# Performance work log

Hardware: AMD Instinct MI355X
Metric: run time of the kernel (lower is better)

Reference implementation:

```python
import jax, jax.numpy as jnp
import numpy as np

N, I, H = 32, 64, 128
B, T = 16, 256


def setup_inputs() -> dict:
    key = jax.random.key(0)
    k1, k2, k3, k4, k5 = jax.random.split(key, 5)
    stdv = 1.0 / np.sqrt(H)
    x = jax.random.normal(k1, (B, T, N * I), dtype=jnp.float32)
    h0 = jnp.zeros((1, B, N * H), dtype=jnp.float32)
    c0 = jnp.zeros((1, B, N * H), dtype=jnp.float32)
    # Block-diagonal weights stored as batched per-block matrices.
    # weight_ih block i is [4H, I], weight_hh block i is [4H, H].
    weight_ih = jax.random.uniform(k2, (N, 4 * H, I), jnp.float32, -stdv, stdv)
    weight_hh = jax.random.uniform(k3, (N, 4 * H, H), jnp.float32, -stdv, stdv)
    bias_ih = jax.random.uniform(k4, (N, 4 * H), jnp.float32, -stdv, stdv)
    bias_hh = jax.random.uniform(k5, (N, 4 * H), jnp.float32, -stdv, stdv)
    return {"x": x, "h0": h0, "c0": c0, "weight_ih": weight_ih,
            "weight_hh": weight_hh, "bias_ih": bias_ih, "bias_hh": bias_hh}


def _wide_lstm(x, h0, c0, weight_ih, weight_hh, bias_ih, bias_hh):
    b, t, _ = x.shape
    xb = x.reshape(b, t, N, I)
    # Precompute input-to-gate projections for all timesteps: [B,T,N,4H]
    gates_x = jnp.einsum('btni,ngi->btng', xb, weight_ih) + bias_ih
    h_t = h0[0].reshape(b, N, H)
    c_t = c0[0].reshape(b, N, H)

    def step(carry, gx_t):
        h, c = carry
        gates_h = jnp.einsum('bnh,ngh->bng', h, weight_hh) + bias_hh
        gates = gx_t + gates_h  # [B,N,4H]
        i_g = jax.nn.sigmoid(gates[..., 0 * H:1 * H])
        f_g = jax.nn.sigmoid(gates[..., 1 * H:2 * H])
        g_g = jnp.tanh(gates[..., 2 * H:3 * H])
        o_g = jax.nn.sigmoid(gates[..., 3 * H:4 * H])
        c_new = f_g * c + i_g * g_g
        h_new = o_g * jnp.tanh(c_new)
        return (h_new, c_new), h_new

    (h_n, c_n), outs = jax.lax.scan(step, (h_t, c_t),
                                    jnp.swapaxes(gates_x, 0, 1))  # scan over T
    output = jnp.swapaxes(outs, 0, 1).reshape(b, t, N * H)
    return output, h_n.reshape(1, b, N * H), c_n.reshape(1, b, N * H)


def reference(x, h0, c0, weight_ih, weight_hh, bias_ih, bias_hh):
    return _wide_lstm(x, h0, c0, weight_ih, weight_hh, bias_ih, bias_hh)
```

## Files before the change

### kernel.cpp

```cpp
#include <hip/hip_runtime.h>
#include <hip/hip_bf16.h>
#include <cstdint>
#include <cstddef>


#define TSTEPS 256

typedef float  f32x4  __attribute__((ext_vector_type(4)));
typedef float  f32x2  __attribute__((ext_vector_type(2)));
typedef __bf16 bf16x8 __attribute__((ext_vector_type(8)));
typedef short  s16x8  __attribute__((ext_vector_type(8)));

union Frag { s16x8 s; bf16x8 b; };

#define KSIG -1.4426950408889634f
#define KTAN  2.8853900817779268f

__device__ __forceinline__ short f2bf(float f) {
  uint32_t u = __builtin_bit_cast(uint32_t, f);
  u += 0x7fffu + ((u >> 16) & 1u);
  return (short)(u >> 16);
}

__device__ __forceinline__ void sync_lds() {
  asm volatile("s_waitcnt lgkmcnt(0)" ::: "memory");
  __builtin_amdgcn_s_barrier();
  asm volatile("" ::: "memory");
}

__device__ __forceinline__ float sig2(float z) {
  return __builtin_amdgcn_rcpf(1.f + __builtin_amdgcn_exp2f(z));
}

__device__ __forceinline__ f32x4 mf(const Frag a, const Frag bb, f32x4 c) {
  return __builtin_amdgcn_mfma_f32_16x16x32_bf16(a.b, bb.b, c, 0, 0, 0);
}

__device__ __forceinline__ float sel4(const f32x4 a, bool m1, bool m2) {
  const float u01 = m1 ? a[1] : a[0];
  const float u23 = m1 ? a[3] : a[2];
  return m2 ? u23 : u01;
}

__global__ __launch_bounds__(1024, 4) void wide_lstm(
    const float* __restrict__ x,   const float* __restrict__ h0,
    const float* __restrict__ c0,  const float* __restrict__ wih,
    const float* __restrict__ whh, const float* __restrict__ bih,
    const float* __restrict__ bhh, float* __restrict__ out)
{
  const int n    = blockIdx.x & 31;
  const int bg   = blockIdx.x >> 5;
  const int tid  = threadIdx.x;
  const int wv   = tid >> 6;
  const int w    = wv & 7;
  const bool isw = (wv < 8);
  const int lane = tid & 63;
  const int col  = lane & 15;
  const int quad = lane >> 4;
  const int b4   = col & 3;
  const int e2   = col >> 2;
  const int hloc = 4 * quad + e2;
  const int hgl  = 16 * w + hloc;
  const int b    = 4 * bg + b4;

  __shared__ alignas(16) short hbuf[2][4 * 144];
  __shared__ alignas(16) short xbuf[2][4 * 96];
  __shared__ alignas(16) float pbuf[8][64][4];

  Frag wfr[3][4];
#pragma unroll
  for (int j = 0; j < 4; ++j) {
    const int g = 128 * j + 16 * w + col;
#pragma unroll
    for (int sl = 0; sl < 3; ++sl) {
      const int s = isw ? sl : sl + 3;
      const int k0 = 32 * s + quad * 8;
      const float* p = (s < 2) ? (wih + (size_t)(n * 512 + g) * 64  + k0)
                               : (whh + (size_t)(n * 512 + g) * 128 + (k0 - 64));
      const f32x4 lo = *(const f32x4*)p;
      const f32x4 hi = *(const f32x4*)(p + 4);
      Frag f;
      f.s[0]=f2bf(lo[0]); f.s[1]=f2bf(lo[1]); f.s[2]=f2bf(lo[2]); f.s[3]=f2bf(lo[3]);
      f.s[4]=f2bf(hi[0]); f.s[5]=f2bf(hi[1]); f.s[6]=f2bf(hi[2]); f.s[7]=f2bf(hi[3]);
      wfr[sl][j] = f;
    }
  }

  const int hoff  = b4 * 144 + quad * 8;
  const int hwoff = b4 * 144 + hgl;
  const int xoff  = b4 * 96  + quad * 8;
  const bool m1 = (e2 & 1), m2 = (e2 & 2);
  const f32x4 kzero = (f32x4){0.f, 0.f, 0.f, 0.f};

  f32x4 cb[4], acpre[4];
  float cg = 0.f, ho = 0.f;
  float* outp = nullptr;
  float xr = 0.f;
  const float* xnext = nullptr;

  if (isw) {
#pragma unroll
    for (int j = 0; j < 4; ++j) {
      const int base = n * 512 + 128 * j + 16 * w + quad * 4;
      const f32x4 b1 = *(const f32x4*)(bih + base);
      const f32x4 b2 = *(const f32x4*)(bhh + base);
#pragma unroll
      for (int r = 0; r < 4; ++r) cb[j][r] = b1[r] + b2[r];
    }
    if (tid < 256) {
      const int bi = tid >> 6, j2 = (tid & 63) * 2;
      const f32x2 hv = *(const f32x2*)(h0 + (size_t)(4 * bg + bi) * 4096 + n * 128 + j2);
      *(uint32_t*)&hbuf[0][bi * 144 + j2] =
          (uint32_t)(uint16_t)f2bf(hv[0]) | ((uint32_t)(uint16_t)f2bf(hv[1]) << 16);
    }
    cg = c0[(size_t)b * 4096 + n * 128 + hgl];
    {
      const float* q = x + (size_t)b * (TSTEPS * 2048) + n * 64 + 8 * quad;
      const f32x4 a0 = *(const f32x4*)q;
      const f32x4 a1 = *(const f32x4*)(q + 4);
      const f32x4 a2 = *(const f32x4*)(q + 32);
      const f32x4 a3 = *(const f32x4*)(q + 36);
      Frag xf0, xf1;
#pragma unroll
      for (int r = 0; r < 4; ++r) {
        xf0.s[r]     = f2bf(a0[r]);
        xf0.s[4 + r] = f2bf(a1[r]);
        xf1.s[r]     = f2bf(a2[r]);
        xf1.s[4 + r] = f2bf(a3[r]);
      }
#pragma unroll
      for (int j = 0; j < 4; ++j)
        acpre[j] = mf(wfr[1][j], xf1, mf(wfr[0][j], xf0, cb[j]));
    }
    outp = out + (size_t)b * (TSTEPS * 4096) + n * 128 + hgl;
  } else if (tid < 768) {
    const int bq = (tid >> 6) & 3;
    const int kq = tid & 63;
    const float* xp = x + (size_t)(4 * bg + bq) * (TSTEPS * 2048) + n * 64 + kq;
    xbuf[1][bq * 96 + kq] = f2bf(xp[2048]);
    xr = xp[2 * 2048];
    xnext = xp + 3 * 2048;
  }
  __syncthreads();

  if (isw) {
#define WSTEP(CUR, NXT, S)                                                   \
  {                                                                          \
    Frag hf0;                                                                \
    hf0.s = *(const s16x8*)&hbuf[CUR][hoff];                                 \
    f32x4 ac1[4];                                                            \
    _Pragma("unroll") for (int j = 0; j < 4; ++j)                            \
      ac1[j] = mf(wfr[2][j], hf0, acpre[j]);                                 \
    float pre[4];                                                            \
    _Pragma("unroll") for (int j = 0; j < 4; ++j)                            \
      pre[j] = sel4(ac1[j], m1, m2);                                         \
    sync_lds();                               \
    const f32x4 vv = *(const f32x4*)&pbuf[w][lane][0];                       \
    pre[0] += vv[0]; pre[1] += vv[1]; pre[2] += vv[2]; pre[3] += vv[3];      \
    const float si = sig2(KSIG * pre[0]);                                    \
    const float sf = sig2(KSIG * pre[1]);                                    \
    const float sg = sig2(KTAN * pre[2]);                                    \
    const float so = sig2(KSIG * pre[3]);                                    \
    float cn = __builtin_fmaf(sf, cg, si);                                   \
    cn = __builtin_fmaf(-2.f, si * sg, cn);                                  \
    cg = cn;                                                                 \
    ho = so * __builtin_fmaf(-2.f, sig2(KTAN * cn), 1.f);                    \
    hbuf[NXT][hwoff] = f2bf(ho);                                             \
    *outp = ho;                                                              \
    outp += 4096;                                                            \
    Frag xg0, xg1;                                                           \
    xg0.s = *(const s16x8*)&xbuf[NXT][xoff];                                 \
    xg1.s = *(const s16x8*)&xbuf[NXT][xoff + 32];                            \
    _Pragma("unroll") for (int j = 0; j < 4; ++j)                            \
      acpre[j] = mf(wfr[0][j], xg0, cb[j]);                                  \
    _Pragma("unroll") for (int j = 0; j < 4; ++j)                            \
      acpre[j] = mf(wfr[1][j], xg1, acpre[j]);                               \
    sync_lds();                                                      \
  }
    for (int t = 0; t < TSTEPS; t += 2) {
      WSTEP(0, 1, t);
      WSTEP(1, 0, t + 1);
    }
#undef WSTEP
    out[16777216 +         (size_t)b * 4096 + n * 128 + hgl] = ho;
    out[16777216 + 65536 + (size_t)b * 4096 + n * 128 + hgl] = cg;
  } else {
    const int sxoff = ((tid >> 6) & 3) * 96 + (tid & 63);
    const bool stg = (tid < 768);
#define VSTEP(CUR, NXT, S)                                                   \
  {                                                                          \
    Frag hf1, hf2, hf3;                                                      \
    hf1.s = *(const s16x8*)&hbuf[CUR][hoff + 32];                            \
    hf2.s = *(const s16x8*)&hbuf[CUR][hoff + 64];                            \
    hf3.s = *(const s16x8*)&hbuf[CUR][hoff + 96];                            \
    if (stg) {                                                               \
      xbuf[CUR][sxoff] = f2bf(xr);                                           \
      if ((S) + 3 < TSTEPS) { xr = *xnext; xnext += 2048; }                  \
    }                                                                        \
    f32x4 ac[4];                                                             \
    _Pragma("unroll") for (int j = 0; j < 4; ++j)                            \
      ac[j] = mf(wfr[0][j], hf1, kzero);                                     \
    _Pragma("unroll") for (int j = 0; j < 4; ++j)                            \
      ac[j] = mf(wfr[1][j], hf2, ac[j]);                                     \
    _Pragma("unroll") for (int j = 0; j < 4; ++j)                            \
      ac[j] = mf(wfr[2][j], hf3, ac[j]);                                     \
    f32x4 vv;                                                                \
    vv[0] = sel4(ac[0], m1, m2);                                             \
    vv[1] = sel4(ac[1], m1, m2);                                             \
    vv[2] = sel4(ac[2], m1, m2);                                             \
    vv[3] = sel4(ac[3], m1, m2);                                             \
    *(f32x4*)&pbuf[w][lane][0] = vv;                                         \
    sync_lds();                                                       \
    sync_lds();                                                      \
  }
    for (int t = 0; t < TSTEPS; t += 2) {
      VSTEP(0, 1, t);
      VSTEP(1, 0, t + 1);
    }
#undef VSTEP
  }
}

extern "C" void kernel_launch(void* const* d_in, const int* in_sizes, int n_in,
                              void* d_out, int out_size, void* d_ws, size_t ws_size,
                              hipStream_t stream) {
  const float* x   = (const float*)d_in[0];
  const float* h0  = (const float*)d_in[1];
  const float* c0  = (const float*)d_in[2];
  const float* wih = (const float*)d_in[3];
  const float* whh = (const float*)d_in[4];
  const float* bih = (const float*)d_in[5];
  const float* bhh = (const float*)d_in[6];
  float* out = (float*)d_out;
  wide_lstm<<<128, 1024, 0, stream>>>(x, h0, c0, wih, whh, bih, bhh, out);
}
```

Before: 267.9 us.

## Precompute input gate projections in a separate GEMM kernel before recurrence

Adds a gx_gemm kernel that computes x·W_ih plus both biases for all timesteps into a workspace buffer. The recurrent kernel then only runs the h·W_hh MFMAs, split evenly between two wave groups, and the helper waves prefetch precomputed gate values four steps ahead. The goal is to take the input projection and x staging off the serial per-step critical path. The cost is an extra kernel launch and a 256 MB fp32 workspace written and read back. The old fused kernel is kept as a fallback when the workspace is too small.

```diff
diff --git a/kernel.cpp b/kernel.cpp
--- a/kernel.cpp
+++ b/kernel.cpp
@@ -42,7 +42,199 @@
   return m2 ? u23 : u01;
 }
 
-__global__ __launch_bounds__(1024, 4) void wide_lstm(
+__global__ __launch_bounds__(512, 2) void gx_gemm(
+    const float* __restrict__ x,   const float* __restrict__ wih,
+    const float* __restrict__ bih, const float* __restrict__ bhh,
+    float* __restrict__ gx)
+{
+  const int n    = blockIdx.x >> 4;
+  const int b    = blockIdx.x & 15;
+  const int tid  = threadIdx.x;
+  const int v    = tid >> 6;
+  const int lane = tid & 63;
+  const int col  = lane & 15;
+  const int quad = lane >> 4;
+
+  Frag wA[4][2];
+#pragma unroll
+  for (int tt = 0; tt < 4; ++tt) {
+    const int g = 128 * (col & 3) + 16 * v + 4 * tt + (col >> 2);
+#pragma unroll
+    for (int s = 0; s < 2; ++s) {
+      const float* p = wih + (size_t)(n * 512 + g) * 64 + 32 * s + quad * 8;
+      const f32x4 lo = *(const f32x4*)p;
+      const f32x4 hi = *(const f32x4*)(p + 4);
+      Frag f;
+      f.s[0]=f2bf(lo[0]); f.s[1]=f2bf(lo[1]); f.s[2]=f2bf(lo[2]); f.s[3]=f2bf(lo[3]);
+      f.s[4]=f2bf(hi[0]); f.s[5]=f2bf(hi[1]); f.s[6]=f2bf(hi[2]); f.s[7]=f2bf(hi[3]);
+      wA[tt][s] = f;
+    }
+  }
+  f32x4 cb[4];
+#pragma unroll
+  for (int tt = 0; tt < 4; ++tt)
+#pragma unroll
+    for (int r = 0; r < 4; ++r) {
+      const int g2 = n * 512 + 128 * r + 16 * v + 4 * tt + quad;
+      cb[tt][r] = bih[g2] + bhh[g2];
+    }
+
+  float* gout = gx + (size_t)(n * 16 + b) * 256 * 512;
+#pragma unroll 2
+  for (int it = 0; it < 16; ++it) {
+    const int t = 16 * it + col;
+    const float* xp = x + ((size_t)b * 256 + t) * 2048 + n * 64;
+    const f32x4 a0 = *(const f32x4*)(xp + 8 * quad);
+    const f32x4 a1 = *(const f32x4*)(xp + 8 * quad + 4);
+    const f32x4 a2 = *(const f32x4*)(xp + 32 + 8 * quad);
+    const f32x4 a3 = *(const f32x4*)(xp + 36 + 8 * quad);
+    Frag xf0, xf1;
+#pragma unroll
+    for (int r = 0; r < 4; ++r) {
+      xf0.s[r]     = f2bf(a0[r]);
+      xf0.s[4 + r] = f2bf(a1[r]);
+      xf1.s[r]     = f2bf(a2[r]);
+      xf1.s[4 + r] = f2bf(a3[r]);
+    }
+#pragma unroll
+    for (int tt = 0; tt < 4; ++tt) {
+      const f32x4 ac = mf(wA[tt][1], xf1, mf(wA[tt][0], xf0, cb[tt]));
+      *(f32x4*)(gout + (size_t)t * 512 + (16 * v + 4 * tt + quad) * 4) = ac;
+    }
+  }
+}
+
+__global__ __launch_bounds__(1024, 2) void wide_lstm_pc(
+    const float* __restrict__ h0,  const float* __restrict__ c0,
+    const float* __restrict__ whh, const float* __restrict__ gx,
+    float* __restrict__ out)
+{
+  const int n    = blockIdx.x & 31;
+  const int bg   = blockIdx.x >> 5;
+  const int tid  = threadIdx.x;
+  const int wv   = tid >> 6;
+  const int w    = wv & 7;
+  const bool isw = (wv < 8);
+  const int lane = tid & 63;
+  const int col  = lane & 15;
+  const int quad = lane >> 4;
+  const int b4   = col & 3;
+  const int e2   = col >> 2;
+  const int hloc = 4 * quad + e2;
+  const int hgl  = 16 * w + hloc;
+  const int b    = 4 * bg + b4;
+
+  __shared__ alignas(16) short hbuf[2][4 * 144];
+  __shared__ alignas(16) float pbuf[8][64][4];
+
+  Frag wfr[2][4];
+#pragma unroll
+  for (int j = 0; j < 4; ++j) {
+    const int g = 128 * j + 16 * w + col;
+#pragma unroll
+    for (int sl = 0; sl < 2; ++sl) {
+      const int k0 = (isw ? 32 * sl : 64 + 32 * sl) + quad * 8;
+      const float* p = whh + (size_t)(n * 512 + g) * 128 + k0;
+      const f32x4 lo = *(const f32x4*)p;
+      const f32x4 hi = *(const f32x4*)(p + 4);
+      Frag f;
+      f.s[0]=f2bf(lo[0]); f.s[1]=f2bf(lo[1]); f.s[2]=f2bf(lo[2]); f.s[3]=f2bf(lo[3]);
+      f.s[4]=f2bf(hi[0]); f.s[5]=f2bf(hi[1]); f.s[6]=f2bf(hi[2]); f.s[7]=f2bf(hi[3]);
+      wfr[sl][j] = f;
+    }
+  }
+
+  const int hoff  = b4 * 144 + quad * 8;
+  const int hwoff = b4 * 144 + hgl;
+  const bool m1 = (e2 & 1), m2 = (e2 & 2);
+  const f32x4 kzero = (f32x4){0.f, 0.f, 0.f, 0.f};
+
+  if (isw) {
+    if (tid < 256) {
+      const int bi = tid >> 6, j2 = (tid & 63) * 2;
+      const f32x2 hv = *(const f32x2*)(h0 + (size_t)(4 * bg + bi) * 4096 + n * 128 + j2);
+      *(uint32_t*)&hbuf[0][bi * 144 + j2] =
+          (uint32_t)(uint16_t)f2bf(hv[0]) | ((uint32_t)(uint16_t)f2bf(hv[1]) << 16);
+    }
+    float cg = c0[(size_t)b * 4096 + n * 128 + hgl];
+    float* outp = out + (size_t)b * (TSTEPS * 4096) + n * 128 + hgl;
+    float ho = 0.f;
+    __syncthreads();
+
+#define WSTEP(CUR, NXT)                                                      \
+  {                                                                          \
+    Frag hf0, hf1;                                                           \
+    hf0.s = *(const s16x8*)&hbuf[CUR][hoff];                                 \
+    hf1.s = *(const s16x8*)&hbuf[CUR][hoff + 32];                            \
+    f32x4 ac1[4];                                                            \
+    _Pragma("unroll") for (int j = 0; j < 4; ++j)                            \
+      ac1[j] = mf(wfr[1][j], hf1, mf(wfr[0][j], hf0, kzero));                \
+    float pre[4];                                                            \
+    _Pragma("unroll") for (int j = 0; j < 4; ++j)                            \
+      pre[j] = sel4(ac1[j], m1, m2);                                         \
+    sync_lds();                      \
+    const f32x4 vv = *(const f32x4*)&pbuf[w][lane][0];                       \
+    pre[0] += vv[0]; pre[1] += vv[1]; pre[2] += vv[2]; pre[3] += vv[3];      \
+    const float si = sig2(KSIG * pre[0]);                                    \
+    const float sf = sig2(KSIG * pre[1]);                                    \
+    const float sg = sig2(KTAN * pre[2]);                                    \
+    const float so = sig2(KSIG * pre[3]);                                    \
+    float cn = __builtin_fmaf(sf, cg, si);                                   \
+    cn = __builtin_fmaf(-2.f, si * sg, cn);                                  \
+    cg = cn;                                                                 \
+    ho = so * __builtin_fmaf(-2.f, sig2(KTAN * cn), 1.f);                    \
+    hbuf[NXT][hwoff] = f2bf(ho);                                             \
+    *outp = ho;                                                              \
+    outp += 4096;                                                            \
+    sync_lds();                                                      \
+  }
+    for (int t = 0; t < TSTEPS; t += 4) {
+      WSTEP(0, 1); WSTEP(1, 0); WSTEP(0, 1); WSTEP(1, 0);
+    }
+#undef WSTEP
+    out[16777216 +         (size_t)b * 4096 + n * 128 + hgl] = ho;
+    out[16777216 + 65536 + (size_t)b * 4096 + n * 128 + hgl] = cg;
+
+  } else {
+    const float* gp = gx + (size_t)(n * 16 + b) * 256 * 512 + hgl * 4;
+    f32x4 g0 = *(const f32x4*)(gp);
+    f32x4 g1 = *(const f32x4*)(gp + 512);
+    f32x4 g2 = *(const f32x4*)(gp + 1024);
+    f32x4 g3 = *(const f32x4*)(gp + 1536);
+    __syncthreads();
+
+#define PSTEP(CUR, NXT, S, GX)                                               \
+  {                                                                          \
+    Frag hf2, hf3;                                                           \
+    hf2.s = *(const s16x8*)&hbuf[CUR][hoff + 64];                            \
+    hf3.s = *(const s16x8*)&hbuf[CUR][hoff + 96];                            \
+    f32x4 ac[4];                                                             \
+    _Pragma("unroll") for (int j = 0; j < 4; ++j)                            \
+      ac[j] = mf(wfr[1][j], hf3, mf(wfr[0][j], hf2, kzero));                 \
+    f32x4 vv;                                                                \
+    vv[0] = sel4(ac[0], m1, m2) + GX[0];                                     \
+    vv[1] = sel4(ac[1], m1, m2) + GX[1];                                     \
+    vv[2] = sel4(ac[2], m1, m2) + GX[2];                                     \
+    vv[3] = sel4(ac[3], m1, m2) + GX[3];                                     \
+    *(f32x4*)&pbuf[w][lane][0] = vv;                                         \
+    {                                                                        \
+      const int tt = ((S) + 4 < TSTEPS) ? (S) + 4 : (TSTEPS - 1);            \
+      GX = *(const f32x4*)(gp + (size_t)tt * 512);                           \
+    }                                                                        \
+    sync_lds();                                                       \
+    sync_lds();                                                      \
+  }
+    for (int t = 0; t < TSTEPS; t += 4) {
+      PSTEP(0, 1, t,     g0);
+      PSTEP(1, 0, t + 1, g1);
+      PSTEP(0, 1, t + 2, g2);
+      PSTEP(1, 0, t + 3, g3);
+    }
+#undef PSTEP
+  }
+}
+
+__global__ __launch_bounds__(1024, 4) void wide_lstm_fb(
     const float* __restrict__ x,   const float* __restrict__ h0,
     const float* __restrict__ c0,  const float* __restrict__ wih,
     const float* __restrict__ whh, const float* __restrict__ bih,
@@ -114,24 +306,6 @@
           (uint32_t)(uint16_t)f2bf(hv[0]) | ((uint32_t)(uint16_t)f2bf(hv[1]) << 16);
     }
     cg = c0[(size_t)b * 4096 + n * 128 + hgl];
-    {
-      const float* q = x + (size_t)b * (TSTEPS * 2048) + n * 64 + 8 * quad;
-      const f32x4 a0 = *(const f32x4*)q;
-      const f32x4 a1 = *(const f32x4*)(q + 4);
-      const f32x4 a2 = *(const f32x4*)(q + 32);
-      const f32x4 a3 = *(const f32x4*)(q + 36);
-      Frag xf0, xf1;
-#pragma unroll
-      for (int r = 0; r < 4; ++r) {
-        xf0.s[r]     = f2bf(a0[r]);
-        xf0.s[4 + r] = f2bf(a1[r]);
-        xf1.s[r]     = f2bf(a2[r]);
-        xf1.s[4 + r] = f2bf(a3[r]);
-      }
-#pragma unroll
-      for (int j = 0; j < 4; ++j)
-        acpre[j] = mf(wfr[1][j], xf1, mf(wfr[0][j], xf0, cb[j]));
-    }
     outp = out + (size_t)b * (TSTEPS * 4096) + n * 128 + hgl;
   } else if (tid < 768) {
     const int bq = (tid >> 6) & 3;
@@ -144,7 +318,7 @@
   __syncthreads();
 
   if (isw) {
-#define WSTEP(CUR, NXT, S)                                                   \
+#define WSTEPF(CUR, NXT, S)                                                  \
   {                                                                          \
     Frag hf0;                                                                \
     hf0.s = *(const s16x8*)&hbuf[CUR][hoff];                                 \
@@ -154,7 +328,7 @@
     float pre[4];                                                            \
     _Pragma("unroll") for (int j = 0; j < 4; ++j)                            \
       pre[j] = sel4(ac1[j], m1, m2);                                         \
-    sync_lds();                               \
+    sync_lds();                                                              \
     const f32x4 vv = *(const f32x4*)&pbuf[w][lane][0];                       \
     pre[0] += vv[0]; pre[1] += vv[1]; pre[2] += vv[2]; pre[3] += vv[3];      \
     const float si = sig2(KSIG * pre[0]);                                    \
@@ -175,19 +349,37 @@
       acpre[j] = mf(wfr[0][j], xg0, cb[j]);                                  \
     _Pragma("unroll") for (int j = 0; j < 4; ++j)                            \
       acpre[j] = mf(wfr[1][j], xg1, acpre[j]);                               \
-    sync_lds();                                                      \
-  }
+    sync_lds();                                                              \
+  }
+    {
+      const float* q = x + (size_t)b * (TSTEPS * 2048) + n * 64 + 8 * quad;
+      const f32x4 a0 = *(const f32x4*)q;
+      const f32x4 a1 = *(const f32x4*)(q + 4);
+      const f32x4 a2 = *(const f32x4*)(q + 32);
+      const f32x4 a3 = *(const f32x4*)(q + 36);
+      Frag xf0, xf1;
+#pragma unroll
+      for (int r = 0; r < 4; ++r) {
+        xf0.s[r]     = f2bf(a0[r]);
+        xf0.s[4 + r] = f2bf(a1[r]);
+        xf1.s[r]     = f2bf(a2[r]);
+        xf1.s[4 + r] = f2bf(a3[r]);
+      }
+#pragma unroll
+      for (int j = 0; j < 4; ++j)
+        acpre[j] = mf(wfr[1][j], xf1, mf(wfr[0][j], xf0, cb[j]));
+    }
     for (int t = 0; t < TSTEPS; t += 2) {
-      WSTEP(0, 1, t);
-      WSTEP(1, 0, t + 1);
-    }
-#undef WSTEP
+      WSTEPF(0, 1, t);
+      WSTEPF(1, 0, t + 1);
+    }
+#undef WSTEPF
     out[16777216 +         (size_t)b * 4096 + n * 128 + hgl] = ho;
     out[16777216 + 65536 + (size_t)b * 4096 + n * 128 + hgl] = cg;
   } else {
     const int sxoff = ((tid >> 6) & 3) * 96 + (tid & 63);
     const bool stg = (tid < 768);
-#define VSTEP(CUR, NXT, S)                                                   \
+#define VSTEPF(CUR, NXT, S)                                                  \
   {                                                                          \
     Frag hf1, hf2, hf3;                                                      \
     hf1.s = *(const s16x8*)&hbuf[CUR][hoff + 32];                            \
@@ -210,14 +402,18 @@
     vv[2] = sel4(ac[2], m1, m2);                                             \
     vv[3] = sel4(ac[3], m1, m2);                                             \
     *(f32x4*)&pbuf[w][lane][0] = vv;                                         \
-    sync_lds();                                                       \
-    sync_lds();                                                      \
-  }
+    sync_lds();                                                              \
+    sync_lds();                                                              \
+  }
+    {
+      const float* q = x + (size_t)b * (TSTEPS * 2048) + n * 64 + 8 * quad;
+      (void)q;
+    }
     for (int t = 0; t < TSTEPS; t += 2) {
-      VSTEP(0, 1, t);
-      VSTEP(1, 0, t + 1);
-    }
-#undef VSTEP
+      VSTEPF(0, 1, t);
+      VSTEPF(1, 0, t + 1);
+    }
+#undef VSTEPF
   }
 }
 
@@ -232,5 +428,12 @@
   const float* bih = (const float*)d_in[5];
   const float* bhh = (const float*)d_in[6];
   float* out = (float*)d_out;
-  wide_lstm<<<128, 1024, 0, stream>>>(x, h0, c0, wih, whh, bih, bhh, out);
-}
+  const size_t need = (size_t)512 * 256 * 512 * 4;
+  if (ws_size >= need && d_ws != nullptr) {
+    float* gxw = (float*)d_ws;
+    gx_gemm<<<512, 512, 0, stream>>>(x, wih, bih, bhh, gxw);
+    wide_lstm_pc<<<128, 1024, 0, stream>>>(h0, c0, whh, gxw, out);
+  } else {
+    wide_lstm_fb<<<128, 1024, 0, stream>>>(x, h0, c0, wih, whh, bih, bhh, out);
+  }
+}
```

After: 328.0 us. 1.22x slower.

## Move input projection to helper waves and rebalance recurrent K-split between wave groups

Applied to the files above, without the earlier changes.

Worker waves now handle only the first half of the recurrent h·W_hh product plus bias. The helper waves take the second half together with the full x·W_ih projection for the next step, loading x directly from global memory into registers one step ahead. This removes the LDS x staging buffer and shortens the serial critical path of the worker waves after each barrier, moving the x MFMA work off that path. In exchange the helper waves carry more per-step work and register pressure, and each of them now loads x itself instead of sharing one staged copy.

```diff
diff --git a/kernel.cpp b/kernel.cpp
--- a/kernel.cpp
+++ b/kernel.cpp
@@ -64,19 +64,21 @@
   const int b    = 4 * bg + b4;
 
   __shared__ alignas(16) short hbuf[2][4 * 144];
-  __shared__ alignas(16) short xbuf[2][4 * 96];
   __shared__ alignas(16) float pbuf[8][64][4];
 
-  Frag wfr[3][4];
+  const int hoff  = b4 * 144 + quad * 8;
+  const int hwoff = b4 * 144 + hgl;
+  const bool m1 = (e2 & 1), m2 = (e2 & 2);
+  const f32x4 kzero = (f32x4){0.f, 0.f, 0.f, 0.f};
+
+  Frag wfr[2][4];
 #pragma unroll
   for (int j = 0; j < 4; ++j) {
     const int g = 128 * j + 16 * w + col;
 #pragma unroll
-    for (int sl = 0; sl < 3; ++sl) {
-      const int s = isw ? sl : sl + 3;
-      const int k0 = 32 * s + quad * 8;
-      const float* p = (s < 2) ? (wih + (size_t)(n * 512 + g) * 64  + k0)
-                               : (whh + (size_t)(n * 512 + g) * 128 + (k0 - 64));
+    for (int sl = 0; sl < 2; ++sl) {
+      const int k0 = (isw ? 32 * sl : 64 + 32 * sl) + quad * 8;
+      const float* p = whh + (size_t)(n * 512 + g) * 128 + k0;
       const f32x4 lo = *(const f32x4*)p;
       const f32x4 hi = *(const f32x4*)(p + 4);
       Frag f;
@@ -86,19 +88,8 @@
     }
   }
 
-  const int hoff  = b4 * 144 + quad * 8;
-  const int hwoff = b4 * 144 + hgl;
-  const int xoff  = b4 * 96  + quad * 8;
-  const bool m1 = (e2 & 1), m2 = (e2 & 2);
-  const f32x4 kzero = (f32x4){0.f, 0.f, 0.f, 0.f};
-
-  f32x4 cb[4], acpre[4];
-  float cg = 0.f, ho = 0.f;
-  float* outp = nullptr;
-  float xr = 0.f;
-  const float* xnext = nullptr;
-
   if (isw) {
+    f32x4 cb[4];
 #pragma unroll
     for (int j = 0; j < 4; ++j) {
       const int base = n * 512 + 128 * j + 16 * w + quad * 4;
@@ -113,48 +104,23 @@
       *(uint32_t*)&hbuf[0][bi * 144 + j2] =
           (uint32_t)(uint16_t)f2bf(hv[0]) | ((uint32_t)(uint16_t)f2bf(hv[1]) << 16);
     }
-    cg = c0[(size_t)b * 4096 + n * 128 + hgl];
-    {
-      const float* q = x + (size_t)b * (TSTEPS * 2048) + n * 64 + 8 * quad;
-      const f32x4 a0 = *(const f32x4*)q;
-      const f32x4 a1 = *(const f32x4*)(q + 4);
-      const f32x4 a2 = *(const f32x4*)(q + 32);
-      const f32x4 a3 = *(const f32x4*)(q + 36);
-      Frag xf0, xf1;
-#pragma unroll
-      for (int r = 0; r < 4; ++r) {
-        xf0.s[r]     = f2bf(a0[r]);
-        xf0.s[4 + r] = f2bf(a1[r]);
-        xf1.s[r]     = f2bf(a2[r]);
-        xf1.s[4 + r] = f2bf(a3[r]);
-      }
-#pragma unroll
-      for (int j = 0; j < 4; ++j)
-        acpre[j] = mf(wfr[1][j], xf1, mf(wfr[0][j], xf0, cb[j]));
-    }
-    outp = out + (size_t)b * (TSTEPS * 4096) + n * 128 + hgl;
-  } else if (tid < 768) {
-    const int bq = (tid >> 6) & 3;
-    const int kq = tid & 63;
-    const float* xp = x + (size_t)(4 * bg + bq) * (TSTEPS * 2048) + n * 64 + kq;
-    xbuf[1][bq * 96 + kq] = f2bf(xp[2048]);
-    xr = xp[2 * 2048];
-    xnext = xp + 3 * 2048;
-  }
-  __syncthreads();
-
-  if (isw) {
-#define WSTEP(CUR, NXT, S)                                                   \
+    float cg = c0[(size_t)b * 4096 + n * 128 + hgl];
+    float* outp = out + (size_t)b * (TSTEPS * 4096) + n * 128 + hgl;
+    float ho = 0.f;
+    __syncthreads();
+
+#define WSTEP(CUR, NXT)                                                      \
   {                                                                          \
-    Frag hf0;                                                                \
+    Frag hf0, hf1;                                                           \
     hf0.s = *(const s16x8*)&hbuf[CUR][hoff];                                 \
+    hf1.s = *(const s16x8*)&hbuf[CUR][hoff + 32];                            \
     f32x4 ac1[4];                                                            \
     _Pragma("unroll") for (int j = 0; j < 4; ++j)                            \
-      ac1[j] = mf(wfr[2][j], hf0, acpre[j]);                                 \
+      ac1[j] = mf(wfr[1][j], hf1, mf(wfr[0][j], hf0, cb[j]));                \
     float pre[4];                                                            \
     _Pragma("unroll") for (int j = 0; j < 4; ++j)                            \
       pre[j] = sel4(ac1[j], m1, m2);                                         \
-    sync_lds();                               \
+    sync_lds();           \
     const f32x4 vv = *(const f32x4*)&pbuf[w][lane][0];                       \
     pre[0] += vv[0]; pre[1] += vv[1]; pre[2] += vv[2]; pre[3] += vv[3];      \
     const float si = sig2(KSIG * pre[0]);                                    \
@@ -168,42 +134,68 @@
     hbuf[NXT][hwoff] = f2bf(ho);                                             \
     *outp = ho;                                                              \
     outp += 4096;                                                            \
-    Frag xg0, xg1;                                                           \
-    xg0.s = *(const s16x8*)&xbuf[NXT][xoff];                                 \
-    xg1.s = *(const s16x8*)&xbuf[NXT][xoff + 32];                            \
-    _Pragma("unroll") for (int j = 0; j < 4; ++j)                            \
-      acpre[j] = mf(wfr[0][j], xg0, cb[j]);                                  \
-    _Pragma("unroll") for (int j = 0; j < 4; ++j)                            \
-      acpre[j] = mf(wfr[1][j], xg1, acpre[j]);                               \
     sync_lds();                                                      \
   }
     for (int t = 0; t < TSTEPS; t += 2) {
-      WSTEP(0, 1, t);
-      WSTEP(1, 0, t + 1);
+      WSTEP(0, 1);
+      WSTEP(1, 0);
     }
 #undef WSTEP
     out[16777216 +         (size_t)b * 4096 + n * 128 + hgl] = ho;
     out[16777216 + 65536 + (size_t)b * 4096 + n * 128 + hgl] = cg;
+
   } else {
-    const int sxoff = ((tid >> 6) & 3) * 96 + (tid & 63);
-    const bool stg = (tid < 768);
-#define VSTEP(CUR, NXT, S)                                                   \
+    Frag wfx[2][4];
+#pragma unroll
+    for (int j = 0; j < 4; ++j) {
+      const int g = 128 * j + 16 * w + col;
+#pragma unroll
+      for (int sl = 0; sl < 2; ++sl) {
+        const float* p = wih + (size_t)(n * 512 + g) * 64 + 32 * sl + quad * 8;
+        const f32x4 lo = *(const f32x4*)p;
+        const f32x4 hi = *(const f32x4*)(p + 4);
+        Frag f;
+        f.s[0]=f2bf(lo[0]); f.s[1]=f2bf(lo[1]); f.s[2]=f2bf(lo[2]); f.s[3]=f2bf(lo[3]);
+        f.s[4]=f2bf(hi[0]); f.s[5]=f2bf(hi[1]); f.s[6]=f2bf(hi[2]); f.s[7]=f2bf(hi[3]);
+        wfx[sl][j] = f;
+      }
+    }
+    const float* xb = x + (size_t)b * (TSTEPS * 2048) + n * 64 + 8 * quad;
+
+    f32x4 xacc[4];
+    {
+      const f32x4 a0 = *(const f32x4*)xb;
+      const f32x4 a1 = *(const f32x4*)(xb + 4);
+      const f32x4 a2 = *(const f32x4*)(xb + 32);
+      const f32x4 a3 = *(const f32x4*)(xb + 36);
+      Frag xf0, xf1;
+#pragma unroll
+      for (int r = 0; r < 4; ++r) {
+        xf0.b[r]     = (__bf16)a0[r];
+        xf0.b[4 + r] = (__bf16)a1[r];
+        xf1.b[r]     = (__bf16)a2[r];
+        xf1.b[4 + r] = (__bf16)a3[r];
+      }
+#pragma unroll
+      for (int j = 0; j < 4; ++j)
+        xacc[j] = mf(wfx[1][j], xf1, mf(wfx[0][j], xf0, kzero));
+    }
+    f32x4 rx0, rx1, rx2, rx3;
+    {
+      const float* p1 = xb + 2048;
+      rx0 = *(const f32x4*)p1;        rx1 = *(const f32x4*)(p1 + 4);
+      rx2 = *(const f32x4*)(p1 + 32); rx3 = *(const f32x4*)(p1 + 36);
+    }
+    __syncthreads();
+
+#define PSTEP(CUR, NXT, S)                                                   \
   {                                                                          \
-    Frag hf1, hf2, hf3;                                                      \
-    hf1.s = *(const s16x8*)&hbuf[CUR][hoff + 32];                            \
+    Frag hf2, hf3;                                                           \
     hf2.s = *(const s16x8*)&hbuf[CUR][hoff + 64];                            \
     hf3.s = *(const s16x8*)&hbuf[CUR][hoff + 96];                            \
-    if (stg) {                                                               \
-      xbuf[CUR][sxoff] = f2bf(xr);                                           \
-      if ((S) + 3 < TSTEPS) { xr = *xnext; xnext += 2048; }                  \
-    }                                                                        \
     f32x4 ac[4];                                                             \
     _Pragma("unroll") for (int j = 0; j < 4; ++j)                            \
-      ac[j] = mf(wfr[0][j], hf1, kzero);                                     \
-    _Pragma("unroll") for (int j = 0; j < 4; ++j)                            \
-      ac[j] = mf(wfr[1][j], hf2, ac[j]);                                     \
-    _Pragma("unroll") for (int j = 0; j < 4; ++j)                            \
-      ac[j] = mf(wfr[2][j], hf3, ac[j]);                                     \
+      ac[j] = mf(wfr[1][j], hf3, mf(wfr[0][j], hf2, xacc[j]));               \
     f32x4 vv;                                                                \
     vv[0] = sel4(ac[0], m1, m2);                                             \
     vv[1] = sel4(ac[1], m1, m2);                                             \
@@ -211,13 +203,30 @@
     vv[3] = sel4(ac[3], m1, m2);                                             \
     *(f32x4*)&pbuf[w][lane][0] = vv;                                         \
     sync_lds();                                                       \
+    Frag xg0, xg1;                                                           \
+    _Pragma("unroll") for (int r = 0; r < 4; ++r) {                          \
+      xg0.b[r]     = (__bf16)rx0[r];                                         \
+      xg0.b[4 + r] = (__bf16)rx1[r];                                         \
+      xg1.b[r]     = (__bf16)rx2[r];                                         \
+      xg1.b[4 + r] = (__bf16)rx3[r];                                         \
+    }                                                                        \
+    _Pragma("unroll") for (int j = 0; j < 4; ++j)                            \
+      xacc[j] = mf(wfx[0][j], xg0, kzero);                                   \
+    _Pragma("unroll") for (int j = 0; j < 4; ++j)                            \
+      xacc[j] = mf(wfx[1][j], xg1, xacc[j]);                                 \
+    {                                                                        \
+      const int tt = ((S) + 2 < TSTEPS) ? (S) + 2 : (TSTEPS - 1);            \
+      const float* p2 = xb + (size_t)tt * 2048;                              \
+      rx0 = *(const f32x4*)p2;        rx1 = *(const f32x4*)(p2 + 4);         \
+      rx2 = *(const f32x4*)(p2 + 32); rx3 = *(const f32x4*)(p2 + 36);        \
+    }                                                                        \
     sync_lds();                                                      \
   }
     for (int t = 0; t < TSTEPS; t += 2) {
-      VSTEP(0, 1, t);
-      VSTEP(1, 0, t + 1);
-    }
-#undef VSTEP
+      PSTEP(0, 1, t);
+      PSTEP(1, 0, t + 1);
+    }
+#undef PSTEP
   }
 }
 
```

New measurement: 479.8 us. 79.1% more time.
